# Kernel optimization log

Hardware: AMD Instinct MI355X
Metric: run time of the kernel (lower is better)

Reference implementation:

```python
import jax, jax.numpy as jnp
import numpy as np

B, D, H, W, C = 2, 8, 128, 128, 64
HEADS, DH = 4, 16
EPS = 1e-12  # torch F.normalize eps


def setup_inputs() -> dict:
    key = jax.random.key(0)
    ks = jax.random.split(key, 8)
    rn = lambda k, shp, s: jax.random.normal(k, shp, jnp.float32) * s
    return {
        "x_in": rn(ks[0], (B, D, H, W, C), 1.0),
        "Wq": rn(ks[1], (C, HEADS * DH), 0.05),
        "Wk": rn(ks[2], (C, HEADS * DH), 0.05),
        "Wv": rn(ks[3], (C, HEADS * DH), 0.05),
        "rescale": jnp.ones((HEADS, 1, 1), jnp.float32),
        "Wproj": rn(ks[4], (HEADS * DH, C), 0.05),
        "bproj": jnp.zeros((C,), jnp.float32),
        "Wpos1": rn(ks[5], (C, 1, 3, 3, 3), 0.1),
        "Wpos2": rn(ks[6], (C, 1, 3, 3, 3), 0.1),
    }


def _l2norm(x):
    # torch F.normalize(p=2, dim=-1): x / max(||x||, eps)
    return x / jnp.maximum(jnp.linalg.norm(x, axis=-1, keepdims=True), EPS)


def _dwconv3d(x, w):
    # depthwise Conv3d, kernel 3, stride 1, padding 1, groups = channels
    return jax.lax.conv_general_dilated(
        x, w, (1, 1, 1), 'SAME',
        dimension_numbers=('NCDHW', 'OIDHW', 'NCDHW'),
        feature_group_count=w.shape[0])


def reference(x_in, Wq, Wk, Wv, rescale, Wproj, bproj, Wpos1, Wpos2):
    b, d, h, w, c = x_in.shape
    n = d * h * w
    x = x_in.reshape(b, n, c)
    v_inp = x @ Wv                                   # [b, n, heads*dh]
    # [b, heads, dh, n] layout (attention over channel dim)
    q = jnp.transpose((x @ Wq).reshape(b, n, HEADS, DH), (0, 2, 3, 1))
    k = jnp.transpose((x @ Wk).reshape(b, n, HEADS, DH), (0, 2, 3, 1))
    v = jnp.transpose(v_inp.reshape(b, n, HEADS, DH), (0, 2, 3, 1))
    q = _l2norm(q)
    k = _l2norm(k)
    attn = jnp.einsum('bhdn,bhen->bhde', k, q) * rescale  # [b, heads, dh, dh]
    attn = jax.nn.softmax(attn, axis=-1)
    out = jnp.einsum('bhde,bhen->bhdn', attn, v)          # [b, heads, dh, n]
    out = jnp.transpose(out, (0, 3, 1, 2)).reshape(b, n, HEADS * DH)
    out_c = (out @ Wproj + bproj).reshape(b, d, h, w, c)
    # positional branch: depthwise conv -> GELU -> depthwise conv on v_inp
    vv = jnp.transpose(v_inp.reshape(b, d, h, w, c), (0, 4, 1, 2, 3))  # NCDHW
    p = _dwconv3d(vv, Wpos1)
    p = jax.nn.gelu(p, approximate=False)
    p = _dwconv3d(p, Wpos2)
    out_p = jnp.transpose(p, (0, 2, 3, 4, 1))
    return out_c + out_p
```

## Files before the change

### kernel.cpp

```cpp
#include <hip/hip_runtime.h>
#include <math.h>

#define DD 8
#define HH 128
#define WW2 128
#define NPT 131072
#define NTOT 262144
#define NBK 16

typedef __attribute__((ext_vector_type(8))) short short8;
typedef __attribute__((ext_vector_type(4))) float f32x4;
typedef __attribute__((ext_vector_type(4))) unsigned short u16x4;
typedef __attribute__((ext_vector_type(8))) unsigned short u16x8;
typedef unsigned short u16;

static const size_t OFF_P1  = 0;
static const size_t OFF_P2  = 33554432;
static const size_t OFF_V   = 67108864;
static const size_t OFF_PW  = 100663296;
static const size_t OFF_PM  = 100687872;
static const size_t OFF_FLAG= 100704256;
static const size_t OFF_CW  = 100704768;
static const size_t OFF_PART= 134217728;
static const size_t OFF_VP  = 150994944;
#define SP_F    0
#define WQ_F    131072
#define WK_F    135168
#define CW_WPROJ 0
#define CW_WPOS1 4096
#define CW_WPOS2 5824
#define CW_RESC  7552
#define CW_BPROJ 7556

__device__ __forceinline__ float bf2f(u16 u){
  unsigned int x = ((unsigned int)u) << 16;
  return __builtin_bit_cast(float, x);
}
__device__ __forceinline__ u16 f2bf(float f){
  unsigned int x = __builtin_bit_cast(unsigned int, f);
  unsigned int r = (x + 0x7fffu + ((x >> 16) & 1u)) >> 16;
  return (u16)r;
}

__device__ __forceinline__ float fgelu(float o){
  float z  = o * 0.70710678118654752f;
  float az = fabsf(z);
  float t1 = __builtin_amdgcn_rcpf(fmaf(0.3275911f, az, 1.f));
  float poly = t1 * fmaf(t1, fmaf(t1, fmaf(t1, fmaf(t1, 1.061405429f,
               -1.453152027f), 1.421413741f), -0.284496736f), 0.254829592f);
  float ex = __expf(-z * z);
  float er = 1.f - poly * ex;
  er = (z < 0.f) ? -er : er;
  return 0.5f * o * (1.f + er);
}

__device__ __forceinline__ int probe_isf32(const void* x, int t){
  u16 u = ((const u16*)x)[2 * (t & 63)];
  int e = (u >> 7) & 0xFF;
  int plaus = (u == 0) || (u == 0x8000u) || (e >= 100 && e <= 130);
  unsigned long long m = __ballot(plaus);
  return (__popcll(m) < 48) ? 1 : 0;
}

__global__ __launch_bounds__(256) void k_prep(const void* __restrict__ x,
    const void* __restrict__ Wproj, const void* __restrict__ rescale,
    const void* __restrict__ bproj, const void* __restrict__ Wpos1,
    const void* __restrict__ Wpos2, const void* __restrict__ Wq,
    const void* __restrict__ Wk, const void* __restrict__ Wv,
    int* __restrict__ flag, float* __restrict__ cw, float* __restrict__ gpart,
    u16* __restrict__ packW){
  __shared__ int sflag;
  int t = threadIdx.x, blk = blockIdx.x;
  if (t < 64){
    int f = probe_isf32(x, t);
    if (t == 0) sflag = f;
  }
  __syncthreads();
  int isf32 = sflag;
  if (blk < 32){
    for (int i = blk * 4096 + t; i < (blk + 1) * 4096; i += 256)
      gpart[i] = 0.f;
    if (blk == 0){
      if (t == 0) *flag = isf32;
      auto conv = [&](const void* src, float* dst, int n){
        for (int i = t; i < n; i += 256)
          dst[i] = isf32 ? ((const float*)src)[i] : bf2f(((const u16*)src)[i]);
      };
      conv(Wproj, cw + CW_WPROJ, 4096);
      conv(Wpos1, cw + CW_WPOS1, 1728);
      conv(Wpos2, cw + CW_WPOS2, 1728);
      conv(rescale, cw + CW_RESC, 4);
      conv(bproj,   cw + CW_BPROJ, 64);
      conv(Wq, gpart + WQ_F, 4096);
      conv(Wk, gpart + WK_F, 4096);
    }
  } else {
    int o = (blk - 32) * 256 + t;
    int f = o >> 9, l = (o >> 3) & 63, j = o & 7;
    int tt = f >> 1, s = f & 1;
    int k = s * 32 + (l >> 4) * 8 + j;
    int n = tt * 16 + (l & 15);
    int idx = k * 64 + n;
    float val = isf32 ? ((const float*)Wv)[idx] : bf2f(((const u16*)Wv)[idx]);
    packW[o] = f2bf(val);
  }
}

__device__ __forceinline__ short8 ld8_adapt(const void* p, size_t idx, int isf32){
  if (!isf32) return *(const short8*)((const u16*)p + idx);
  const float4* f = (const float4*)((const float*)p + idx);
  float4 u = f[0], v2 = f[1];
  short8 r;
  r[0] = (short)f2bf(u.x);  r[1] = (short)f2bf(u.y);
  r[2] = (short)f2bf(u.z);  r[3] = (short)f2bf(u.w);
  r[4] = (short)f2bf(v2.x); r[5] = (short)f2bf(v2.y);
  r[6] = (short)f2bf(v2.z); r[7] = (short)f2bf(v2.w);
  return r;
}

__global__ __launch_bounds__(512) void k_qkv(const void* __restrict__ x,
                                             const int* __restrict__ flag,
                                             const u16* __restrict__ packW,
                                             u16* __restrict__ vT,
                                             u16* __restrict__ vP,
                                             float* __restrict__ Sp){
  __shared__ u16 sXT[64][136];
  __shared__ u16 sV[8][16][72];
  int isf32 = *flag;
  int wave = threadIdx.x >> 6, lane = threadIdx.x & 63;
  int m = lane & 15, quad = lane >> 4;
  const short8* bw = (const short8*)packW;
  short8 bv[8];
#pragma unroll
  for (int f = 0; f < 8; f++) bv[f] = bw[f * 64 + lane];
  int c1 = wave >> 1, c2p = (wave & 1) * 2;
  f32x4 aS[2];
  aS[0] = (f32x4)(0.f); aS[1] = (f32x4)(0.f);

  int pbase = blockIdx.x * 256;
  int b = pbase >> 17;

  for (int s = 0; s < 2; s++){
    int p0 = pbase + s * 128 + wave * 16;
    size_t rowbase = (size_t)(p0 + m) * 64;
    short8 a0 = ld8_adapt(x, rowbase + quad * 8, isf32);
    short8 a1 = ld8_adapt(x, rowbase + 32 + quad * 8, isf32);
    f32x4 av[4];
#pragma unroll
    for (int t = 0; t < 4; t++) av[t] = (f32x4)(0.f);
#pragma unroll
    for (int t = 0; t < 4; t++){
      av[t] = __builtin_amdgcn_mfma_f32_16x16x32_bf16(a0, bv[t * 2 + 0], av[t], 0, 0, 0);
      av[t] = __builtin_amdgcn_mfma_f32_16x16x32_bf16(a1, bv[t * 2 + 1], av[t], 0, 0, 0);
    }
    int nloc = p0 & (NPT - 1);
#pragma unroll
    for (int t = 0; t < 4; t++){
      u16x4 pk;
#pragma unroll
      for (int r = 0; r < 4; r++) pk[r] = f2bf(av[t][r]);
      *(u16x4*)(vT + ((size_t)(b * 64 + t * 16 + m)) * NPT + nloc + quad * 4) = pk;
#pragma unroll
      for (int r = 0; r < 4; r++) sV[wave][quad * 4 + r][t * 16 + m] = pk[r];
    }
    {
      int pr = lane >> 3, ch8 = (lane & 7) * 8;
      u16x8 v0 = *(const u16x8*)&sV[wave][pr][ch8];
      *(u16x8*)(vP + (size_t)(p0 + pr) * 64 + ch8) = v0;
      u16x8 v1 = *(const u16x8*)&sV[wave][8 + pr][ch8];
      *(u16x8*)(vP + (size_t)(p0 + 8 + pr) * 64 + ch8) = v1;
    }
    if (s) __syncthreads();
#pragma unroll
    for (int j = 0; j < 8; j++){
      sXT[quad * 8 + j][wave * 16 + m]      = (u16)a0[j];
      sXT[32 + quad * 8 + j][wave * 16 + m] = (u16)a1[j];
    }
    __syncthreads();
#pragma unroll
    for (int ks = 0; ks < 4; ks++){
      short8 fA  = *(const short8*)&sXT[c1 * 16 + m][ks * 32 + quad * 8];
      short8 fB0 = *(const short8*)&sXT[(c2p + 0) * 16 + m][ks * 32 + quad * 8];
      short8 fB1 = *(const short8*)&sXT[(c2p + 1) * 16 + m][ks * 32 + quad * 8];
      aS[0] = __builtin_amdgcn_mfma_f32_16x16x32_bf16(fA, fB0, aS[0], 0, 0, 0);
      aS[1] = __builtin_amdgcn_mfma_f32_16x16x32_bf16(fA, fB1, aS[1], 0, 0, 0);
    }
  }
  int bk = blockIdx.x & (NBK - 1);
  float* Sb = Sp + (size_t)(bk * 2 + b) * 4096;
#pragma unroll
  for (int tt = 0; tt < 2; tt++)
#pragma unroll
    for (int r = 0; r < 4; r++)
      atomicAdd(&Sb[(c1 * 16 + quad * 4 + r) * 64 + (c2p + tt) * 16 + m], aS[tt][r]);
}

__global__ __launch_bounds__(256) void k_attn_h(const float* __restrict__ Sp,
    const float* __restrict__ wqk, const float* __restrict__ cw,
    u16* __restrict__ packM){
  __shared__ float sS[64 * 65];
  __shared__ float sWh[1024];
  __shared__ float sT[1024];
  __shared__ float sG[256];
  __shared__ float sA[256];
  __shared__ float sNq[16], sNk[16];
  int blk = blockIdx.x, t = threadIdx.x;
  int b = blk >> 2, h = blk & 3;
  for (int i = t; i < 4096; i += 256){
    float s = 0.f;
#pragma unroll
    for (int bk = 0; bk < NBK; bk++) s += Sp[(size_t)(bk * 2 + b) * 4096 + i];
    sS[(i >> 6) * 65 + (i & 63)] = s;
  }
  for (int i = t; i < 1024; i += 256)
    sWh[i] = wqk[(i >> 4) * 64 + h * 16 + (i & 15)];
  __syncthreads();
  int cc = t & 63, eg = t >> 6;
  {
    float a0 = 0.f, a1 = 0.f, a2 = 0.f, a3 = 0.f;
    for (int c2 = 0; c2 < 64; c2++){
      float sv = sS[cc * 65 + c2];
      a0 = fmaf(sv, sWh[c2 * 16 + eg * 4 + 0], a0);
      a1 = fmaf(sv, sWh[c2 * 16 + eg * 4 + 1], a1);
      a2 = fmaf(sv, sWh[c2 * 16 + eg * 4 + 2], a2);
      a3 = fmaf(sv, sWh[c2 * 16 + eg * 4 + 3], a3);
    }
    sT[cc * 16 + eg * 4 + 0] = a0;
    sT[cc * 16 + eg * 4 + 1] = a1;
    sT[cc * 16 + eg * 4 + 2] = a2;
    sT[cc * 16 + eg * 4 + 3] = a3;
  }
  __syncthreads();
  if (t < 16){
    float a = 0.f;
    for (int c = 0; c < 64; c++) a += sWh[c * 16 + t] * sT[c * 16 + t];
    sNq[t] = a;
  }
  __syncthreads();
  for (int i = t; i < 1024; i += 256)
    sWh[i] = wqk[4096 + (i >> 4) * 64 + h * 16 + (i & 15)];
  __syncthreads();
  {
    int d = t >> 4, e = t & 15;
    float a = 0.f;
    for (int c = 0; c < 64; c++) a += sWh[c * 16 + d] * sT[c * 16 + e];
    sG[d * 16 + e] = a;
  }
  __syncthreads();
  {
    float a0 = 0.f, a1 = 0.f, a2 = 0.f, a3 = 0.f;
    for (int c2 = 0; c2 < 64; c2++){
      float sv = sS[cc * 65 + c2];
      a0 = fmaf(sv, sWh[c2 * 16 + eg * 4 + 0], a0);
      a1 = fmaf(sv, sWh[c2 * 16 + eg * 4 + 1], a1);
      a2 = fmaf(sv, sWh[c2 * 16 + eg * 4 + 2], a2);
      a3 = fmaf(sv, sWh[c2 * 16 + eg * 4 + 3], a3);
    }
    __syncthreads();
    sT[cc * 16 + eg * 4 + 0] = a0;
    sT[cc * 16 + eg * 4 + 1] = a1;
    sT[cc * 16 + eg * 4 + 2] = a2;
    sT[cc * 16 + eg * 4 + 3] = a3;
  }
  __syncthreads();
  if (t < 16){
    float a = 0.f;
    for (int c = 0; c < 64; c++) a += sWh[c * 16 + t] * sT[c * 16 + t];
    sNk[t] = a;
  }
  __syncthreads();
  for (int i = t; i < 1024; i += 256)
    sT[i] = cw[CW_WPROJ + (h * 16 + (i >> 6)) * 64 + (i & 63)];
  if (t < 16){
    int d = t;
    float nk = fmaxf(sqrtf(sNk[d]), 1e-12f);
    float rs = cw[CW_RESC + h];
    float lg[16]; float mx = -1e30f;
#pragma unroll
    for (int e = 0; e < 16; e++){
      float nq = fmaxf(sqrtf(sNq[e]), 1e-12f);
      float L = sG[d * 16 + e] / (nk * nq) * rs;
      lg[e] = L; mx = fmaxf(mx, L);
    }
    float sum = 0.f;
#pragma unroll
    for (int e = 0; e < 16; e++){ lg[e] = expf(lg[e] - mx); sum += lg[e]; }
    float inv = 1.f / sum;
#pragma unroll
    for (int e = 0; e < 16; e++) sA[d * 16 + e] = lg[e] * inv;
  }
  __syncthreads();
#pragma unroll
  for (int q = 0; q < 4; q++){
    int i = q * 256 + t;
    int t4 = i >> 8, lhi = (i >> 7) & 1, llo = (i >> 3) & 15, j = i & 7;
    int e = lhi * 8 + j, c = t4 * 16 + llo;
    float acc = 0.f;
#pragma unroll
    for (int d = 0; d < 16; d++) acc += sA[d * 16 + e] * sT[d * 64 + c];
    int f = t4 * 2 + (h >> 1);
    int l = (2 * (h & 1) + lhi) * 16 + llo;
    packM[b * 4096 + f * 512 + l * 8 + j] = f2bf(acc);
  }
}

template <bool GELU>
__global__ __launch_bounds__(256, 4) void k_dwconv(const u16* __restrict__ src,
    const float* __restrict__ wpos, u16* __restrict__ dst){
  int xi = threadIdx.x & 15, ty = threadIdx.x >> 4;
  int zp = ty >> 2, yq = ty & 3;
  int x0 = xi * 8;
  int c  = blockIdx.x;
  int y0 = blockIdx.y * 8 + yq * 2;
  int b  = blockIdx.z;
  int z0 = zp * 2;
  const float* wg = wpos + c * 27;
  float w27[27];
#pragma unroll
  for (int i = 0; i < 27; i++) w27[i] = wg[i];
  const u16* plane = src + (size_t)(b * 64 + c) * NPT;

  short8 raw[16];
  const short8 zz8 = (short8)0;
#pragma unroll
  for (int iz = 0; iz < 4; iz++){
    int zz = z0 - 1 + iz;
    int zc = zz < 0 ? 0 : (zz > DD - 1 ? DD - 1 : zz);
    int zv = (zz == zc);
#pragma unroll
    for (int iy = 0; iy < 4; iy++){
      int yy = y0 - 1 + iy;
      int yc = yy < 0 ? 0 : (yy > HH - 1 ? HH - 1 : yy);
      short8 v = *(const short8*)(plane + zc * 16384 + yc * 128 + x0);
      raw[iz * 4 + iy] = (zv && yy == yc) ? v : zz8;
    }
  }

  float acc[2][2][8];
#pragma unroll
  for (int dz = 0; dz < 2; dz++)
#pragma unroll
    for (int dy = 0; dy < 2; dy++)
#pragma unroll
      for (int xx = 0; xx < 8; xx++) acc[dz][dy][xx] = 0.f;

#pragma unroll
  for (int iz = 0; iz < 4; iz++){
#pragma unroll
    for (int iy = 0; iy < 4; iy++){
      short8 mid = raw[iz * 4 + iy];
      float row[10];
#pragma unroll
      for (int e = 0; e < 8; e++) row[1 + e] = bf2f((u16)mid[e]);
      float lf = __shfl_up(row[8], 1);
      float rg = __shfl_down(row[1], 1);
      row[0] = (xi > 0)  ? lf : 0.f;
      row[9] = (xi < 15) ? rg : 0.f;
#pragma unroll
      for (int dzi = 0; dzi < 2; dzi++){
        int kd = iz - dzi;
        if (kd < 0 || kd > 2) continue;
#pragma unroll
        for (int dyi = 0; dyi < 2; dyi++){
          int kh = iy - dyi;
          if (kh < 0 || kh > 2) continue;
#pragma unroll
          for (int kw = 0; kw < 3; kw++){
            float w = w27[kd * 9 + kh * 3 + kw];
#pragma unroll
            for (int xx = 0; xx < 8; xx++)
              acc[dzi][dyi][xx] = fmaf(row[xx + kw], w, acc[dzi][dyi][xx]);
          }
        }
      }
    }
  }
#pragma unroll
  for (int dzi = 0; dzi < 2; dzi++){
    int zo = z0 + dzi;
#pragma unroll
    for (int dyi = 0; dyi < 2; dyi++){
      int yo = y0 + dyi;
      u16x8 pk;
#pragma unroll
      for (int xx = 0; xx < 8; xx++){
        float o = acc[dzi][dyi][xx];
        if (GELU) o = fgelu(o);
        pk[xx] = f2bf(o);
      }
      *(u16x8*)(dst + (size_t)(b * 64 + c) * NPT + zo * 16384 + yo * 128 + x0) = pk;
    }
  }
}

__global__ __launch_bounds__(256) void k_final(const u16* __restrict__ vP,
                                               const u16* __restrict__ packM,
                                               const float* __restrict__ bprojf,
                                               const u16* __restrict__ p2T,
                                               float* __restrict__ out){
  int wave = threadIdx.x >> 6, lane = threadIdx.x & 63;
  int m = lane & 15, quad = lane >> 4;
  int p0 = blockIdx.x * 64 + wave * 16;
  int b = p0 >> 17;
  int nloc = p0 & (NPT - 1);
  size_t rowbase = (size_t)(p0 + m) * 64;
  short8 a0 = *(const short8*)(vP + rowbase + quad * 8);
  short8 a1 = *(const short8*)(vP + rowbase + 32 + quad * 8);
  const short8* bm = (const short8*)(packM + (size_t)b * 4096);
  f32x4 acc[4];
#pragma unroll
  for (int t = 0; t < 4; t++) acc[t] = (f32x4)(0.f);
#pragma unroll
  for (int t = 0; t < 4; t++){
    short8 b0 = bm[(t * 2 + 0) * 64 + lane];
    short8 b1 = bm[(t * 2 + 1) * 64 + lane];
    acc[t] = __builtin_amdgcn_mfma_f32_16x16x32_bf16(a0, b0, acc[t], 0, 0, 0);
    acc[t] = __builtin_amdgcn_mfma_f32_16x16x32_bf16(a1, b1, acc[t], 0, 0, 0);
  }
#pragma unroll
  for (int t = 0; t < 4; t++){
    int c = t * 16 + m;
    float bias = bprojf[c];
    u16x4 pv = *(const u16x4*)(p2T + (size_t)(b * 64 + c) * NPT + nloc + quad * 4);
#pragma unroll
    for (int r = 0; r < 4; r++){
      size_t p = (size_t)p0 + quad * 4 + r;
      out[p * 64 + c] = acc[t][r] + bias + bf2f(pv[r]);
    }
  }
}

extern "C" void kernel_launch(void* const* d_in, const int* in_sizes, int n_in,
                              void* d_out, int out_size, void* d_ws, size_t ws_size,
                              hipStream_t stream){
  (void)in_sizes; (void)n_in; (void)out_size; (void)ws_size;
  const void* x      = d_in[0];
  const void* Wq     = d_in[1];
  const void* Wk     = d_in[2];
  const void* Wv     = d_in[3];
  const void* rescale= d_in[4];
  const void* Wproj  = d_in[5];
  const void* bproj  = d_in[6];
  const void* Wpos1  = d_in[7];
  const void* Wpos2  = d_in[8];

  char* ws = (char*)d_ws;
  u16* p1T   = (u16*)(ws + OFF_P1);
  u16* p2T   = (u16*)(ws + OFF_P2);
  u16* vT    = (u16*)(ws + OFF_V);
  u16* vP    = (u16*)(ws + OFF_VP);
  u16* packW = (u16*)(ws + OFF_PW);
  u16* packM = (u16*)(ws + OFF_PM);
  int* flag  = (int*)(ws + OFF_FLAG);
  float* cw  = (float*)(ws + OFF_CW);
  float* part= (float*)(ws + OFF_PART);
  float* Sp  = part + SP_F;
  float* wqk = part + WQ_F;
  float* out = (float*)d_out;

  k_prep<<<48, 256, 0, stream>>>(x, Wproj, rescale, bproj, Wpos1, Wpos2, Wq, Wk, Wv,
                                 flag, cw, Sp, packW);
  k_qkv<<<NTOT / 256, 512, 0, stream>>>(x, flag, packW, vT, vP, Sp);
  k_attn_h<<<8, 256, 0, stream>>>(Sp, wqk, cw, packM);
  k_dwconv<true><<<dim3(64, 16, 2), 256, 0, stream>>>(vT, cw + CW_WPOS1, p1T);
  k_dwconv<false><<<dim3(64, 16, 2), 256, 0, stream>>>(p1T, cw + CW_WPOS2, p2T);
  k_final<<<NTOT / 64, 256, 0, stream>>>(vP, packM, cw + CW_BPROJ, p2T, out);
}
```

Measured before the change: 267.6 us.

## Restructure qkv Gram accumulation per block and coalesce final output stores via LDS

k_qkv now runs 4 waves per block over 512 positions in 8 steps, each wave accumulating a full 16x64 row strip of the x^T x Gram matrix, so the grid is half as large and there are fewer global atomics in total. k_final stages the p2T tile and the output tile in shared memory, so the strided 2-byte p2T reads and the scattered fp32 output writes become coalesced vector accesses. The cost is extra barriers and more shared memory per block. The qkv loop is also longer and serial, which gives less parallelism per block.

```diff
diff --git a/kernel.cpp b/kernel.cpp
--- a/kernel.cpp
+++ b/kernel.cpp
@@ -118,14 +118,14 @@
   return r;
 }
 
-__global__ __launch_bounds__(512) void k_qkv(const void* __restrict__ x,
+__global__ __launch_bounds__(256) void k_qkv(const void* __restrict__ x,
                                              const int* __restrict__ flag,
                                              const u16* __restrict__ packW,
                                              u16* __restrict__ vT,
                                              u16* __restrict__ vP,
                                              float* __restrict__ Sp){
-  __shared__ u16 sXT[64][136];
-  __shared__ u16 sV[8][16][72];
+  __shared__ u16 sXT[64][72];
+  __shared__ u16 sV[4][16][72];
   int isf32 = *flag;
   int wave = threadIdx.x >> 6, lane = threadIdx.x & 63;
   int m = lane & 15, quad = lane >> 4;
@@ -133,15 +133,16 @@
   short8 bv[8];
 #pragma unroll
   for (int f = 0; f < 8; f++) bv[f] = bw[f * 64 + lane];
-  int c1 = wave >> 1, c2p = (wave & 1) * 2;
-  f32x4 aS[2];
-  aS[0] = (f32x4)(0.f); aS[1] = (f32x4)(0.f);
-
-  int pbase = blockIdx.x * 256;
+  int c1 = wave;
+  f32x4 aS[4];
+#pragma unroll
+  for (int i = 0; i < 4; i++) aS[i] = (f32x4)(0.f);
+
+  int pbase = blockIdx.x * 512;
   int b = pbase >> 17;
 
-  for (int s = 0; s < 2; s++){
-    int p0 = pbase + s * 128 + wave * 16;
+  for (int s = 0; s < 8; s++){
+    int p0 = pbase + s * 64 + wave * 16;
     size_t rowbase = (size_t)(p0 + m) * 64;
     short8 a0 = ld8_adapt(x, rowbase + quad * 8, isf32);
     short8 a1 = ld8_adapt(x, rowbase + 32 + quad * 8, isf32);
@@ -178,21 +179,22 @@
     }
     __syncthreads();
 #pragma unroll
-    for (int ks = 0; ks < 4; ks++){
-      short8 fA  = *(const short8*)&sXT[c1 * 16 + m][ks * 32 + quad * 8];
-      short8 fB0 = *(const short8*)&sXT[(c2p + 0) * 16 + m][ks * 32 + quad * 8];
-      short8 fB1 = *(const short8*)&sXT[(c2p + 1) * 16 + m][ks * 32 + quad * 8];
-      aS[0] = __builtin_amdgcn_mfma_f32_16x16x32_bf16(fA, fB0, aS[0], 0, 0, 0);
-      aS[1] = __builtin_amdgcn_mfma_f32_16x16x32_bf16(fA, fB1, aS[1], 0, 0, 0);
+    for (int ks = 0; ks < 2; ks++){
+      short8 fA = *(const short8*)&sXT[c1 * 16 + m][ks * 32 + quad * 8];
+#pragma unroll
+      for (int c2 = 0; c2 < 4; c2++){
+        short8 fB = *(const short8*)&sXT[c2 * 16 + m][ks * 32 + quad * 8];
+        aS[c2] = __builtin_amdgcn_mfma_f32_16x16x32_bf16(fA, fB, aS[c2], 0, 0, 0);
+      }
     }
   }
   int bk = blockIdx.x & (NBK - 1);
   float* Sb = Sp + (size_t)(bk * 2 + b) * 4096;
 #pragma unroll
-  for (int tt = 0; tt < 2; tt++)
+  for (int c2 = 0; c2 < 4; c2++)
 #pragma unroll
     for (int r = 0; r < 4; r++)
-      atomicAdd(&Sb[(c1 * 16 + quad * 4 + r) * 64 + (c2p + tt) * 16 + m], aS[tt][r]);
+      atomicAdd(&Sb[(c1 * 16 + quad * 4 + r) * 64 + c2 * 16 + m], aS[c2][r]);
 }
 
 __global__ __launch_bounds__(256) void k_attn_h(const float* __restrict__ Sp,
@@ -398,11 +400,23 @@
                                                const float* __restrict__ bprojf,
                                                const u16* __restrict__ p2T,
                                                float* __restrict__ out){
-  int wave = threadIdx.x >> 6, lane = threadIdx.x & 63;
+  __shared__ u16 sP2[64][72];
+  __shared__ float sOut[64][68];
+  int tid = threadIdx.x;
+  int wave = tid >> 6, lane = tid & 63;
   int m = lane & 15, quad = lane >> 4;
-  int p0 = blockIdx.x * 64 + wave * 16;
-  int b = p0 >> 17;
-  int nloc = p0 & (NPT - 1);
+  int pbase = blockIdx.x * 64;
+  int b = pbase >> 17;
+  int nloc = pbase & (NPT - 1);
+  {
+    int c = tid >> 2, po = (tid & 3) * 16;
+    const u16* src = p2T + (size_t)(b * 64 + c) * NPT + nloc + po;
+    u16x8 v0 = *(const u16x8*)src;
+    u16x8 v1 = *(const u16x8*)(src + 8);
+    *(u16x8*)&sP2[c][po]     = v0;
+    *(u16x8*)&sP2[c][po + 8] = v1;
+  }
+  int p0 = pbase + wave * 16;
   size_t rowbase = (size_t)(p0 + m) * 64;
   short8 a0 = *(const short8*)(vP + rowbase + quad * 8);
   short8 a1 = *(const short8*)(vP + rowbase + 32 + quad * 8);
@@ -417,16 +431,25 @@
     acc[t] = __builtin_amdgcn_mfma_f32_16x16x32_bf16(a0, b0, acc[t], 0, 0, 0);
     acc[t] = __builtin_amdgcn_mfma_f32_16x16x32_bf16(a1, b1, acc[t], 0, 0, 0);
   }
+  __syncthreads();
 #pragma unroll
   for (int t = 0; t < 4; t++){
     int c = t * 16 + m;
     float bias = bprojf[c];
-    u16x4 pv = *(const u16x4*)(p2T + (size_t)(b * 64 + c) * NPT + nloc + quad * 4);
 #pragma unroll
     for (int r = 0; r < 4; r++){
-      size_t p = (size_t)p0 + quad * 4 + r;
-      out[p * 64 + c] = acc[t][r] + bias + bf2f(pv[r]);
-    }
+      int lp = wave * 16 + quad * 4 + r;
+      sOut[lp][c] = acc[t][r] + bias + bf2f(sP2[c][lp]);
+    }
+  }
+  __syncthreads();
+  int hi = tid >> 4, lo = tid & 15;
+#pragma unroll
+  for (int k = 0; k < 4; k++){
+    int pos = k * 16 + hi;
+    int c0  = lo * 4;
+    float4 v = *(const float4*)&sOut[pos][c0];
+    *(float4*)(out + (size_t)(pbase + pos) * 64 + c0) = v;
   }
 }
 
@@ -460,7 +483,7 @@
 
   k_prep<<<48, 256, 0, stream>>>(x, Wproj, rescale, bproj, Wpos1, Wpos2, Wq, Wk, Wv,
                                  flag, cw, Sp, packW);
-  k_qkv<<<NTOT / 256, 512, 0, stream>>>(x, flag, packW, vT, vP, Sp);
+  k_qkv<<<NTOT / 512, 256, 0, stream>>>(x, flag, packW, vT, vP, Sp);
   k_attn_h<<<8, 256, 0, stream>>>(Sp, wqk, cw, packM);
   k_dwconv<true><<<dim3(64, 16, 2), 256, 0, stream>>>(vT, cw + CW_WPOS1, p1T);
   k_dwconv<false><<<dim3(64, 16, 2), 256, 0, stream>>>(p1T, cw + CW_WPOS2, p2T);
```

Measured after the change: 251.7 us. -5.9%, faster.
